# Kernel tuning notes

Hardware: AMD Instinct MI355X
Metric: run time of the kernel (lower is better)

## Reference

```python
import jax, jax.numpy as jnp
import numpy as np

B, D, H = 4096, 32, 1024  # batch, in_out_dim, hidden width


def setup_inputs() -> dict:
    key = jax.random.key(0)
    ks = jax.random.split(key, 10)

    def lin_w(k, shape, fan_in):
        bound = 1.0 / np.sqrt(fan_in)
        return jax.random.uniform(k, shape, jnp.float32, -bound, bound)

    return {
        "t": jax.random.uniform(ks[0], (1,), jnp.float32),
        "z": jax.random.normal(ks[1], (B, D), jnp.float32),
        "W0": lin_w(ks[2], (H, D + 1), D + 1),
        "b0": lin_w(ks[3], (H,), D + 1),
        "W1": lin_w(ks[4], (H, H), H),
        "b1": lin_w(ks[5], (H,), H),
        "W2": lin_w(ks[6], (H, H), H),
        "b2": lin_w(ks[7], (H,), H),
        "W3": lin_w(ks[8], (D, H), H),
        "b3": lin_w(ks[9], (D,), H),
    }


def _mlp(v, params):
    # Linear -> Tanh chain, final Linear (torch convention y = x @ W.T + b)
    for W, b in params[:-1]:
        v = jnp.tanh(v @ W.T + b)
    W, b = params[-1]
    return v @ W.T + b


def reference(t, z, W0, b0, W1, b1, W2, b2, W3, b3):
    bsz, d = z.shape
    tt = jnp.broadcast_to(t.reshape(-1), (bsz,))  # check_t: repeat scalar t
    params = [(W0, b0), (W1, b1), (W2, b2), (W3, b3)]

    def f(zz):  # [B, D] -> [B, D]
        v = jnp.concatenate([zz, tt[:, None]], axis=1)  # [B, D+1]
        return _mlp(v, params)

    out = f(z)

    # Exact Jacobian trace via d forward-mode JVPs (replaces the per-dim
    # autograd.grad loop in trace_df_dz with a single vmapped JVP batch).
    eye = jnp.eye(d, dtype=z.dtype)

    def jvp_i(e):
        return jax.jvp(f, (z,), (jnp.broadcast_to(e, z.shape),))[1]  # [B, D]

    tang = jax.vmap(jvp_i)(eye)            # [D, B, D]
    trace = jnp.einsum("ibi->b", tang)     # sum_i df_i/dz_i per sample
    divv = -trace
    return out, divv[:, None]
```

## Files before the change

kernel.cpp:

```cpp
#include <hip/hip_runtime.h>
#include <hip/hip_bf16.h>
#include <stdint.h>


using bf  = __hip_bfloat16;
using bf2 = __hip_bfloat162;
typedef __attribute__((ext_vector_type(8))) short bf16x8;
typedef __attribute__((ext_vector_type(4))) float f32x4;

__device__ __forceinline__ float b2f(bf x)    { return __bfloat162float(x); }
__device__ __forceinline__ bf    f2b(float x) { return __float2bfloat16(x); }

__device__ __forceinline__ void gld16(const void* g, void* l) {
  __builtin_amdgcn_global_load_lds((const __attribute__((address_space(1))) void*)g,
                                   (__attribute__((address_space(3))) void*)l,
                                   16, 0, 0);
}

__device__ __forceinline__ void conv_body(int blk, const float* __restrict__ src,
                                          bf* __restrict__ dst, int n4) {
  const int i = blk * 256 + threadIdx.x;
  if (i >= n4) return;
  float4 v = ((const float4*)src)[i];
  bf2* d = (bf2*)(dst + (size_t)i * 4);
  d[0] = __float22bfloat162_rn(make_float2(v.x, v.y));
  d[1] = __float22bfloat162_rn(make_float2(v.z, v.w));
}

__device__ __forceinline__ void w0t_body(int blk, const float* __restrict__ W0,
                                         bf* __restrict__ W0T) {
  const int idx = blk * 256 + threadIdx.x;
  const int i = idx >> 10, q = idx & 1023;
  W0T[idx] = f2b(W0[q * 33 + i]);
}

__global__ __launch_bounds__(256) void prep_k(const float* __restrict__ z,
                                              const float* __restrict__ tin,
                                              const float* __restrict__ W0,
                                              const float* __restrict__ b0,
                                              const float* __restrict__ W1,
                                              const float* __restrict__ W2,
                                              const float* __restrict__ W3,
                                              bf* __restrict__ h0,
                                              bf* __restrict__ W0T,
                                              bf* __restrict__ W1b,
                                              bf* __restrict__ W2b,
                                              bf* __restrict__ W3b,
                                              float* __restrict__ out2) {
  __shared__ float zs[32 * 33];
  const int f = blockIdx.x, t = threadIdx.x;
  if (f < 128) {
    const int s0 = f * 32;
    for (int j = t; j < 1024; j += 256) {
      const int s = j >> 5, k = j & 31;
      zs[s * 33 + k] = z[(size_t)(s0 + s) * 32 + k];
    }
    if (t < 32) zs[t * 33 + 32] = tin[0];
    __syncthreads();
#pragma unroll 1
    for (int rep = 0; rep < 4; ++rep) {
      const int hh = rep * 256 + t;
      const float* wr = W0 + (size_t)hh * 33;
      float wv[33];
#pragma unroll
      for (int k = 0; k < 33; ++k) wv[k] = wr[k];
      const float bv = b0[hh];
#pragma unroll 1
      for (int s = 0; s < 32; ++s) {
        float acc = bv;
#pragma unroll
        for (int k = 0; k < 33; ++k) acc += wv[k] * zs[s * 33 + k];
        h0[(size_t)(s0 + s) * 1024 + hh] = f2b(tanhf(acc));
      }
    }
  } else if (f < 1152) {
    conv_body(f - 128, W1, W1b, 262144);
  } else if (f < 2176) {
    conv_body(f - 1152, W2, W2b, 262144);
  } else if (f < 2208) {
    conv_body(f - 2176, W3, W3b, 8192);
  } else if (f < 2336) {
    w0t_body(f - 2208, W0, W0T);
  } else {
#pragma unroll
    for (int u = 0; u < 16; ++u) out2[u * 256 + t] = 0.f;
  }
}

__device__ __forceinline__ void gemm_core(bf* As, bf* Bs,
                                          const bf* __restrict__ A,
                                          const bf* __restrict__ B,
                                          size_t m0, size_t n0,
                                          f32x4 (&acc)[8][4]) {
  constexpr int K = 1024;
  const int t = threadIdx.x, l = t & 63, w = t >> 6;
  const int wm = w >> 1, wn = w & 1;
  const int r15 = l & 15, q4 = l >> 4, sw = r15 & 7;

  const int lrow = l >> 3;
  const int lseg = (l & 7) ^ lrow;
  const bf* asrc[8]; bf* alds[8];
  const bf* bsrc[4]; bf* blds[4];
#pragma unroll
  for (int u = 0; u < 8; ++u) {
    const int row = w * 64 + u * 8 + lrow;
    asrc[u] = A + (m0 + row) * K + lseg * 8;
    alds[u] = As + (size_t)(w * 64 + u * 8) * 64;
  }
#pragma unroll
  for (int u = 0; u < 4; ++u) {
    const int row = w * 32 + u * 8 + lrow;
    bsrc[u] = B + (n0 + row) * K + lseg * 8;
    blds[u] = Bs + (size_t)(w * 32 + u * 8) * 64;
  }

#pragma unroll 1
  for (int k0 = 0; k0 < K; k0 += 64) {
#pragma unroll
    for (int u = 0; u < 8; ++u) gld16(asrc[u] + k0, alds[u]);
#pragma unroll
    for (int u = 0; u < 4; ++u) gld16(bsrc[u] + k0, blds[u]);
    __syncthreads();
#pragma unroll
    for (int kk = 0; kk < 2; ++kk) {
      const int sa = (kk * 4 + q4) ^ sw;
      bf16x8 af[8], bfr[4];
#pragma unroll
      for (int i = 0; i < 8; ++i)
        af[i] = *(const bf16x8*)(As + (wm * 128 + i * 16 + r15) * 64 + sa * 8);
#pragma unroll
      for (int j = 0; j < 4; ++j)
        bfr[j] = *(const bf16x8*)(Bs + (wn * 64 + j * 16 + r15) * 64 + sa * 8);
#pragma unroll
      for (int mi = 0; mi < 8; ++mi)
#pragma unroll
        for (int ni = 0; ni < 4; ++ni)
          acc[mi][ni] = __builtin_amdgcn_mfma_f32_16x16x32_bf16(af[mi], bfr[ni], acc[mi][ni], 0, 0, 0);
    }
    __syncthreads();
  }
}

__global__ __launch_bounds__(256, 2) void gemm_fwd(const bf* __restrict__ A,
                                                   const bf* __restrict__ W,
                                                   const float* __restrict__ bias,
                                                   bf* __restrict__ H) {
  constexpr int N = 1024;
  __shared__ __align__(16) bf As[256 * 64];
  __shared__ __align__(16) bf Bs[128 * 64];
  const int t = threadIdx.x, l = t & 63, w = t >> 6;
  const int wm = w >> 1, wn = w & 1;
  const int f = blockIdx.x;
  const int n_t = (f >> 3) & 7, m_t = (f & 7) + 8 * (f >> 6);
  const size_t m0 = (size_t)m_t * 256, n0 = (size_t)n_t * 128;
  const int r15 = l & 15, q4 = l >> 4;
  f32x4 acc[8][4] = {};
  gemm_core(As, Bs, A, W, m0, n0, acc);
#pragma unroll
  for (int ni = 0; ni < 4; ++ni) {
    const int n = (int)n0 + wn * 64 + ni * 16 + r15;
    const float bv = bias[n];
#pragma unroll
    for (int mi = 0; mi < 8; ++mi)
#pragma unroll
      for (int r = 0; r < 4; ++r) {
        const size_t m = m0 + wm * 128 + mi * 16 + q4 * 4 + r;
        H[m * N + n] = f2b(tanhf(acc[mi][ni][r] + bv));
      }
  }
}

__global__ __launch_bounds__(256) void fwd3_k(const bf* __restrict__ h2,
                                              const bf* __restrict__ W3b,
                                              const float* __restrict__ b3,
                                              float* __restrict__ out) {
  __shared__ __align__(16) bf hs[8 * 1024];
  const int t = threadIdx.x;
  const size_t bb = (size_t)blockIdx.x * 8;
  const uint4* src = (const uint4*)(h2 + bb * 1024);
  uint4* dv = (uint4*)hs;
#pragma unroll
  for (int j = 0; j < 4; ++j) dv[j * 256 + t] = src[j * 256 + t];
  __syncthreads();
  const int i = t & 31, bl = t >> 5;
  const bf2* hr = (const bf2*)(hs + bl * 1024);
  const bf2* wr = (const bf2*)(W3b + (size_t)i * 1024);
  float s = 0.f;
#pragma unroll 8
  for (int k2 = 0; k2 < 512; ++k2) {
    float2 a = __bfloat1622float2(hr[k2]);
    float2 c = __bfloat1622float2(wr[k2]);
    s += a.x * c.x + a.y * c.y;
  }
  out[(bb + bl) * 32 + i] = s + b3[i];
}

__global__ __launch_bounds__(256) void t0_k(const bf* __restrict__ h0c,
                                            const bf* __restrict__ W0T,
                                            bf* __restrict__ T0) {
  const int idx = blockIdx.x * 256 + threadIdx.x;
  const int m = idx >> 6, seg = idx & 63;
  const int b = m >> 5, i = m & 31;
  const bf2* hp = (const bf2*)(h0c + (size_t)b * 1024 + seg * 16);
  const bf2* wp = (const bf2*)(W0T + (size_t)i * 1024 + seg * 16);
  bf2* dp = (bf2*)(T0 + (size_t)m * 1024 + seg * 16);
#pragma unroll
  for (int u = 0; u < 8; ++u) {
    float2 h = __bfloat1622float2(hp[u]);
    float2 w = __bfloat1622float2(wp[u]);
    float2 r;
    r.x = (1.f - h.x * h.x) * w.x;
    r.y = (1.f - h.y * h.y) * w.y;
    dp[u] = __float22bfloat162_rn(r);
  }
}

__global__ __launch_bounds__(256, 2) void gemm_jvp1(const bf* __restrict__ T0,
                                                    const bf* __restrict__ W1b,
                                                    const bf* __restrict__ h1c,
                                                    bf* __restrict__ T1) {
  constexpr int N = 1024;
  __shared__ __align__(16) bf As[256 * 64];
  __shared__ __align__(16) bf Bs[128 * 64];
  const int t = threadIdx.x, l = t & 63, w = t >> 6;
  const int wm = w >> 1, wn = w & 1;
  const int f = blockIdx.x;
  const int n_t = (f >> 3) & 7, m_t = (f & 7) + 8 * (f >> 6);
  const size_t m0 = (size_t)m_t * 256, n0 = (size_t)n_t * 128;
  const int r15 = l & 15, q4 = l >> 4;
  f32x4 acc[8][4] = {};
  gemm_core(As, Bs, T0, W1b, m0, n0, acc);
  const int bbase = (int)((m0 + wm * 128) >> 5);
#pragma unroll
  for (int ni = 0; ni < 4; ++ni) {
    const int n = (int)n0 + wn * 64 + ni * 16 + r15;
    float a1v[4];
#pragma unroll
    for (int s = 0; s < 4; ++s) {
      const float hv = b2f(h1c[(size_t)(bbase + s) * 1024 + n]);
      a1v[s] = 1.f - hv * hv;
    }
#pragma unroll
    for (int mi = 0; mi < 8; ++mi)
#pragma unroll
      for (int r = 0; r < 4; ++r) {
        const size_t m = m0 + wm * 128 + mi * 16 + q4 * 4 + r;
        T1[m * N + n] = f2b(a1v[mi >> 1] * acc[mi][ni][r]);
      }
  }
}

__global__ __launch_bounds__(256, 2) void gemm_jvp2(const bf* __restrict__ T1,
                                                    const bf* __restrict__ W2b,
                                                    const bf* __restrict__ W3b,
                                                    const bf* __restrict__ h2c,
                                                    float* __restrict__ out2c) {
  __shared__ __align__(16) bf As[256 * 64];
  __shared__ __align__(16) bf Bs[128 * 64];
  const int t = threadIdx.x, l = t & 63, w = t >> 6;
  const int wm = w >> 1, wn = w & 1;
  const int f = blockIdx.x;
  const int n_t = (f >> 3) & 7, m_t = (f & 7) + 8 * (f >> 6);
  const size_t m0 = (size_t)m_t * 256, n0 = (size_t)n_t * 128;
  const int r15 = l & 15, q4 = l >> 4;
  f32x4 acc[8][4] = {};
  gemm_core(As, Bs, T1, W2b, m0, n0, acc);
  const int bbase = (int)((m0 + wm * 128) >> 5);
  float part[4] = {0.f, 0.f, 0.f, 0.f};
#pragma unroll
  for (int ni = 0; ni < 4; ++ni) {
    const int n = (int)n0 + wn * 64 + ni * 16 + r15;
    float a2v[4];
#pragma unroll
    for (int s = 0; s < 4; ++s) {
      const float hv = b2f(h2c[(size_t)(bbase + s) * 1024 + n]);
      a2v[s] = 1.f - hv * hv;
    }
#pragma unroll
    for (int mi = 0; mi < 8; ++mi) {
      const int isel = mi >> 1;
#pragma unroll
      for (int r = 0; r < 4; ++r) {
        const int mm = wm * 128 + mi * 16 + q4 * 4 + r;
        part[isel] += b2f(W3b[(size_t)(mm & 31) * 1024 + n]) * a2v[isel] * acc[mi][ni][r];
      }
    }
  }
#pragma unroll
  for (int off = 32; off > 0; off >>= 1) {
#pragma unroll
    for (int s = 0; s < 4; ++s) part[s] += __shfl_down(part[s], off);
  }
  if (l == 0) {
#pragma unroll
    for (int s = 0; s < 4; ++s) atomicAdd(out2c + bbase + s, -part[s]);
  }
}

extern "C" void kernel_launch(void* const* d_in, const int* in_sizes, int n_in,
                              void* d_out, int out_size, void* d_ws, size_t ws_size,
                              hipStream_t stream) {
  const float* tin = (const float*)d_in[0];
  const float* z   = (const float*)d_in[1];
  const float* W0  = (const float*)d_in[2];
  const float* b0  = (const float*)d_in[3];
  const float* W1  = (const float*)d_in[4];
  const float* b1  = (const float*)d_in[5];
  const float* W2  = (const float*)d_in[6];
  const float* b2  = (const float*)d_in[7];
  const float* W3  = (const float*)d_in[8];
  const float* b3  = (const float*)d_in[9];
  float* out = (float*)d_out;
  float* out2 = out + 131072;
  (void)in_sizes; (void)n_in; (void)out_size;

  char* ws = (char*)d_ws;
  size_t off = 0;
  auto take = [&](size_t bytes) {
    char* p = ws + off;
    off = (off + bytes + 255) & ~(size_t)255;
    return p;
  };
  bf* h0   = (bf*)take((size_t)4096 * 1024 * 2);
  bf* h1   = (bf*)take((size_t)4096 * 1024 * 2);
  bf* h2   = (bf*)take((size_t)4096 * 1024 * 2);
  bf* W0T  = (bf*)take((size_t)32 * 1024 * 2);
  bf* W1b  = (bf*)take((size_t)1024 * 1024 * 2);
  bf* W2b  = (bf*)take((size_t)1024 * 1024 * 2);
  bf* W3b  = (bf*)take((size_t)32 * 1024 * 2);
  const size_t avail = (ws_size > off) ? (ws_size - off) : 0;
  int NB = 4096;
  while (NB > 256 && 2 * (size_t)NB * 65536 > avail) NB >>= 1;
  bf* T0 = (bf*)take((size_t)NB * 65536);
  bf* T1 = (bf*)take((size_t)NB * 65536);

  prep_k<<<dim3(2337), dim3(256), 0, stream>>>(z, tin, W0, b0, W1, W2, W3,
                                               h0, W0T, W1b, W2b, W3b, out2);
  gemm_fwd<<<dim3(128), dim3(256), 0, stream>>>(h0, W1b, b1, h1);
  gemm_fwd<<<dim3(128), dim3(256), 0, stream>>>(h1, W2b, b2, h2);
  fwd3_k<<<dim3(512), dim3(256), 0, stream>>>(h2, W3b, b3, out);
  for (int cb = 0; cb < 4096; cb += NB) {
    t0_k<<<dim3(NB * 8), dim3(256), 0, stream>>>(h0 + (size_t)cb * 1024, W0T, T0);
    gemm_jvp1<<<dim3(NB), dim3(256), 0, stream>>>(
        T0, W1b, h1 + (size_t)cb * 1024, T1);
    gemm_jvp2<<<dim3(NB), dim3(256), 0, stream>>>(
        T1, W2b, W3b, h2 + (size_t)cb * 1024, out2 + cb);
  }
}
```

Baseline: 819.6 us.

## Software-pipeline JVP chunks in one fused launch and shrink forward GEMM tiles

```diff
diff --git a/kernel.cpp b/kernel.cpp
--- a/kernel.cpp
+++ b/kernel.cpp
@@ -32,6 +32,26 @@
   const int idx = blk * 256 + threadIdx.x;
   const int i = idx >> 10, q = idx & 1023;
   W0T[idx] = f2b(W0[q * 33 + i]);
+}
+
+__device__ __forceinline__ void t0_body(int blk, const bf* __restrict__ h0c,
+                                        const bf* __restrict__ W0T,
+                                        bf* __restrict__ T0) {
+  const int idx = blk * 256 + threadIdx.x;
+  const int m = idx >> 6, seg = idx & 63;
+  const int b = m >> 5, i = m & 31;
+  const bf2* hp = (const bf2*)(h0c + (size_t)b * 1024 + seg * 16);
+  const bf2* wp = (const bf2*)(W0T + (size_t)i * 1024 + seg * 16);
+  bf2* dp = (bf2*)(T0 + (size_t)m * 1024 + seg * 16);
+#pragma unroll
+  for (int u = 0; u < 8; ++u) {
+    float2 h = __bfloat1622float2(hp[u]);
+    float2 w = __bfloat1622float2(wp[u]);
+    float2 r;
+    r.x = (1.f - h.x * h.x) * w.x;
+    r.y = (1.f - h.y * h.y) * w.y;
+    dp[u] = __float22bfloat162_rn(r);
+  }
 }
 
 __global__ __launch_bounds__(256) void prep_k(const float* __restrict__ z,
@@ -87,18 +107,18 @@
   }
 }
 
-__device__ __forceinline__ void gemm_core(bf* As, bf* Bs,
-                                          const bf* __restrict__ A,
-                                          const bf* __restrict__ B,
-                                          size_t m0, size_t n0,
-                                          f32x4 (&acc)[8][4]) {
+
+__device__ __forceinline__ void gemm_core256(bf* As, bf* Bs,
+                                             const bf* __restrict__ A,
+                                             const bf* __restrict__ B,
+                                             size_t m0, size_t n0,
+                                             f32x4 (&acc)[8][4]) {
   constexpr int K = 1024;
   const int t = threadIdx.x, l = t & 63, w = t >> 6;
   const int wm = w >> 1, wn = w & 1;
   const int r15 = l & 15, q4 = l >> 4, sw = r15 & 7;
-
-  const int lrow = l >> 3;
-  const int lseg = (l & 7) ^ lrow;
+  const int lrow = l >> 3, lseg = (l & 7) ^ lrow;
+
   const bf* asrc[8]; bf* alds[8];
   const bf* bsrc[4]; bf* blds[4];
 #pragma unroll
@@ -133,6 +153,52 @@
         bfr[j] = *(const bf16x8*)(Bs + (wn * 64 + j * 16 + r15) * 64 + sa * 8);
 #pragma unroll
       for (int mi = 0; mi < 8; ++mi)
+#pragma unroll
+        for (int ni = 0; ni < 4; ++ni)
+          acc[mi][ni] = __builtin_amdgcn_mfma_f32_16x16x32_bf16(af[mi], bfr[ni], acc[mi][ni], 0, 0, 0);
+    }
+    __syncthreads();
+  }
+}
+
+__device__ __forceinline__ void gemm_core128(bf* As, bf* Bs,
+                                             const bf* __restrict__ A,
+                                             const bf* __restrict__ B,
+                                             size_t m0, size_t n0,
+                                             f32x4 (&acc)[4][4]) {
+  constexpr int K = 1024;
+  const int t = threadIdx.x, l = t & 63, w = t >> 6;
+  const int wm = w >> 1, wn = w & 1;
+  const int r15 = l & 15, q4 = l >> 4, sw = r15 & 7;
+  const int lrow = l >> 3, lseg = (l & 7) ^ lrow;
+
+  const bf* asrc[4]; bf* alds[4];
+  const bf* bsrc[4]; bf* blds[4];
+#pragma unroll
+  for (int u = 0; u < 4; ++u) {
+    const int row = w * 32 + u * 8 + lrow;
+    asrc[u] = A + (m0 + row) * K + lseg * 8;
+    alds[u] = As + (size_t)(w * 32 + u * 8) * 64;
+    bsrc[u] = B + (n0 + row) * K + lseg * 8;
+    blds[u] = Bs + (size_t)(w * 32 + u * 8) * 64;
+  }
+
+#pragma unroll 1
+  for (int k0 = 0; k0 < K; k0 += 64) {
+#pragma unroll
+    for (int u = 0; u < 4; ++u) { gld16(asrc[u] + k0, alds[u]); gld16(bsrc[u] + k0, blds[u]); }
+    __syncthreads();
+#pragma unroll
+    for (int kk = 0; kk < 2; ++kk) {
+      const int sa = (kk * 4 + q4) ^ sw;
+      bf16x8 af[4], bfr[4];
+#pragma unroll
+      for (int i = 0; i < 4; ++i) {
+        af[i]  = *(const bf16x8*)(As + (wm * 64 + i * 16 + r15) * 64 + sa * 8);
+        bfr[i] = *(const bf16x8*)(Bs + (wn * 64 + i * 16 + r15) * 64 + sa * 8);
+      }
+#pragma unroll
+      for (int mi = 0; mi < 4; ++mi)
 #pragma unroll
         for (int ni = 0; ni < 4; ++ni)
           acc[mi][ni] = __builtin_amdgcn_mfma_f32_16x16x32_bf16(af[mi], bfr[ni], acc[mi][ni], 0, 0, 0);
@@ -146,25 +212,25 @@
                                                    const float* __restrict__ bias,
                                                    bf* __restrict__ H) {
   constexpr int N = 1024;
-  __shared__ __align__(16) bf As[256 * 64];
+  __shared__ __align__(16) bf As[128 * 64];
   __shared__ __align__(16) bf Bs[128 * 64];
   const int t = threadIdx.x, l = t & 63, w = t >> 6;
   const int wm = w >> 1, wn = w & 1;
   const int f = blockIdx.x;
   const int n_t = (f >> 3) & 7, m_t = (f & 7) + 8 * (f >> 6);
-  const size_t m0 = (size_t)m_t * 256, n0 = (size_t)n_t * 128;
+  const size_t m0 = (size_t)m_t * 128, n0 = (size_t)n_t * 128;
   const int r15 = l & 15, q4 = l >> 4;
-  f32x4 acc[8][4] = {};
-  gemm_core(As, Bs, A, W, m0, n0, acc);
+  f32x4 acc[4][4] = {};
+  gemm_core128(As, Bs, A, W, m0, n0, acc);
 #pragma unroll
   for (int ni = 0; ni < 4; ++ni) {
     const int n = (int)n0 + wn * 64 + ni * 16 + r15;
     const float bv = bias[n];
 #pragma unroll
-    for (int mi = 0; mi < 8; ++mi)
+    for (int mi = 0; mi < 4; ++mi)
 #pragma unroll
       for (int r = 0; r < 4; ++r) {
-        const size_t m = m0 + wm * 128 + mi * 16 + q4 * 4 + r;
+        const size_t m = m0 + wm * 64 + mi * 16 + q4 * 4 + r;
         H[m * N + n] = f2b(tanhf(acc[mi][ni][r] + bv));
       }
   }
@@ -198,102 +264,89 @@
 __global__ __launch_bounds__(256) void t0_k(const bf* __restrict__ h0c,
                                             const bf* __restrict__ W0T,
                                             bf* __restrict__ T0) {
-  const int idx = blockIdx.x * 256 + threadIdx.x;
-  const int m = idx >> 6, seg = idx & 63;
-  const int b = m >> 5, i = m & 31;
-  const bf2* hp = (const bf2*)(h0c + (size_t)b * 1024 + seg * 16);
-  const bf2* wp = (const bf2*)(W0T + (size_t)i * 1024 + seg * 16);
-  bf2* dp = (bf2*)(T0 + (size_t)m * 1024 + seg * 16);
-#pragma unroll
-  for (int u = 0; u < 8; ++u) {
-    float2 h = __bfloat1622float2(hp[u]);
-    float2 w = __bfloat1622float2(wp[u]);
-    float2 r;
-    r.x = (1.f - h.x * h.x) * w.x;
-    r.y = (1.f - h.y * h.y) * w.y;
-    dp[u] = __float22bfloat162_rn(r);
-  }
-}
-
-__global__ __launch_bounds__(256, 2) void gemm_jvp1(const bf* __restrict__ T0,
-                                                    const bf* __restrict__ W1b,
-                                                    const bf* __restrict__ h1c,
-                                                    bf* __restrict__ T1) {
-  constexpr int N = 1024;
-  __shared__ __align__(16) bf As[256 * 64];
-  __shared__ __align__(16) bf Bs[128 * 64];
+  t0_body(blockIdx.x, h0c, W0T, T0);
+}
+
+__global__ __launch_bounds__(256, 2) void jvp_step_k(
+    const bf* __restrict__ T1p, const bf* __restrict__ h2p,
+    float* __restrict__ out2p,
+    const bf* __restrict__ T0c, const bf* __restrict__ h1c,
+    bf* __restrict__ T1c,
+    const bf* __restrict__ h0n, bf* __restrict__ T0n,
+    const bf* __restrict__ W1b, const bf* __restrict__ W2b,
+    const bf* __restrict__ W3b, const bf* __restrict__ W0T,
+    int n2, int n1) {
+  __shared__ __align__(16) bf smem[24576];
+  const int f = blockIdx.x;
   const int t = threadIdx.x, l = t & 63, w = t >> 6;
   const int wm = w >> 1, wn = w & 1;
-  const int f = blockIdx.x;
-  const int n_t = (f >> 3) & 7, m_t = (f & 7) + 8 * (f >> 6);
+  const int r15 = l & 15, q4 = l >> 4;
+
+  if (f >= n2 + n1) {
+    t0_body(f - n2 - n1, h0n, W0T, T0n);
+    return;
+  }
+  int ff, fam;
+  if (n2 > 0 && n1 > 0) { ff = f >> 1; fam = f & 1; }
+  else if (n2 > 0)      { ff = f; fam = 0; }
+  else                  { ff = f; fam = 1; }
+  const int n_t = (ff >> 3) & 7, m_t = (ff & 7) + 8 * (ff >> 6);
   const size_t m0 = (size_t)m_t * 256, n0 = (size_t)n_t * 128;
-  const int r15 = l & 15, q4 = l >> 4;
-  f32x4 acc[8][4] = {};
-  gemm_core(As, Bs, T0, W1b, m0, n0, acc);
-  const int bbase = (int)((m0 + wm * 128) >> 5);
-#pragma unroll
-  for (int ni = 0; ni < 4; ++ni) {
-    const int n = (int)n0 + wn * 64 + ni * 16 + r15;
-    float a1v[4];
-#pragma unroll
-    for (int s = 0; s < 4; ++s) {
-      const float hv = b2f(h1c[(size_t)(bbase + s) * 1024 + n]);
-      a1v[s] = 1.f - hv * hv;
-    }
-#pragma unroll
-    for (int mi = 0; mi < 8; ++mi)
-#pragma unroll
-      for (int r = 0; r < 4; ++r) {
-        const size_t m = m0 + wm * 128 + mi * 16 + q4 * 4 + r;
-        T1[m * N + n] = f2b(a1v[mi >> 1] * acc[mi][ni][r]);
-      }
-  }
-}
-
-__global__ __launch_bounds__(256, 2) void gemm_jvp2(const bf* __restrict__ T1,
-                                                    const bf* __restrict__ W2b,
-                                                    const bf* __restrict__ W3b,
-                                                    const bf* __restrict__ h2c,
-                                                    float* __restrict__ out2c) {
-  __shared__ __align__(16) bf As[256 * 64];
-  __shared__ __align__(16) bf Bs[128 * 64];
-  const int t = threadIdx.x, l = t & 63, w = t >> 6;
-  const int wm = w >> 1, wn = w & 1;
-  const int f = blockIdx.x;
-  const int n_t = (f >> 3) & 7, m_t = (f & 7) + 8 * (f >> 6);
-  const size_t m0 = (size_t)m_t * 256, n0 = (size_t)n_t * 128;
-  const int r15 = l & 15, q4 = l >> 4;
-  f32x4 acc[8][4] = {};
-  gemm_core(As, Bs, T1, W2b, m0, n0, acc);
-  const int bbase = (int)((m0 + wm * 128) >> 5);
-  float part[4] = {0.f, 0.f, 0.f, 0.f};
-#pragma unroll
-  for (int ni = 0; ni < 4; ++ni) {
-    const int n = (int)n0 + wn * 64 + ni * 16 + r15;
-    float a2v[4];
-#pragma unroll
-    for (int s = 0; s < 4; ++s) {
-      const float hv = b2f(h2c[(size_t)(bbase + s) * 1024 + n]);
-      a2v[s] = 1.f - hv * hv;
-    }
-#pragma unroll
-    for (int mi = 0; mi < 8; ++mi) {
-      const int isel = mi >> 1;
-#pragma unroll
-      for (int r = 0; r < 4; ++r) {
-        const int mm = wm * 128 + mi * 16 + q4 * 4 + r;
-        part[isel] += b2f(W3b[(size_t)(mm & 31) * 1024 + n]) * a2v[isel] * acc[mi][ni][r];
-      }
-    }
-  }
-#pragma unroll
-  for (int off = 32; off > 0; off >>= 1) {
-#pragma unroll
-    for (int s = 0; s < 4; ++s) part[s] += __shfl_down(part[s], off);
-  }
-  if (l == 0) {
-#pragma unroll
-    for (int s = 0; s < 4; ++s) atomicAdd(out2c + bbase + s, -part[s]);
+
+  if (fam == 0) {
+    f32x4 acc[8][4] = {};
+    gemm_core256(smem, smem + 16384, T1p, W2b, m0, n0, acc);
+    const int bbase = (int)((m0 + wm * 128) >> 5);
+    float part[4] = {0.f, 0.f, 0.f, 0.f};
+#pragma unroll
+    for (int ni = 0; ni < 4; ++ni) {
+      const int n = (int)n0 + wn * 64 + ni * 16 + r15;
+      float a2v[4];
+#pragma unroll
+      for (int s = 0; s < 4; ++s) {
+        const float hv = b2f(h2p[(size_t)(bbase + s) * 1024 + n]);
+        a2v[s] = 1.f - hv * hv;
+      }
+#pragma unroll
+      for (int mi = 0; mi < 8; ++mi) {
+        const int isel = mi >> 1;
+#pragma unroll
+        for (int r = 0; r < 4; ++r) {
+          const int mm = wm * 128 + mi * 16 + q4 * 4 + r;
+          part[isel] += b2f(W3b[(size_t)(mm & 31) * 1024 + n]) * a2v[isel] * acc[mi][ni][r];
+        }
+      }
+    }
+#pragma unroll
+    for (int off2 = 32; off2 > 0; off2 >>= 1) {
+#pragma unroll
+      for (int s = 0; s < 4; ++s) part[s] += __shfl_down(part[s], off2);
+    }
+    if (l == 0) {
+#pragma unroll
+      for (int s = 0; s < 4; ++s) atomicAdd(out2p + bbase + s, -part[s]);
+    }
+  } else {
+    f32x4 acc[8][4] = {};
+    gemm_core256(smem, smem + 16384, T0c, W1b, m0, n0, acc);
+    const int bbase = (int)((m0 + wm * 128) >> 5);
+#pragma unroll
+    for (int ni = 0; ni < 4; ++ni) {
+      const int n = (int)n0 + wn * 64 + ni * 16 + r15;
+      float a1v[4];
+#pragma unroll
+      for (int s = 0; s < 4; ++s) {
+        const float hv = b2f(h1c[(size_t)(bbase + s) * 1024 + n]);
+        a1v[s] = 1.f - hv * hv;
+      }
+#pragma unroll
+      for (int mi = 0; mi < 8; ++mi)
+#pragma unroll
+        for (int r = 0; r < 4; ++r) {
+          const size_t m = m0 + wm * 128 + mi * 16 + q4 * 4 + r;
+          T1c[m * 1024 + n] = f2b(a1v[mi >> 1] * acc[mi][ni][r]);
+        }
+    }
   }
 }
 
@@ -329,21 +382,42 @@
   bf* W2b  = (bf*)take((size_t)1024 * 1024 * 2);
   bf* W3b  = (bf*)take((size_t)32 * 1024 * 2);
   const size_t avail = (ws_size > off) ? (ws_size - off) : 0;
-  int NB = 4096;
-  while (NB > 256 && 2 * (size_t)NB * 65536 > avail) NB >>= 1;
-  bf* T0 = (bf*)take((size_t)NB * 65536);
-  bf* T1 = (bf*)take((size_t)NB * 65536);
+  int NB = 1024;
+  while (NB > 256 && 4 * (size_t)NB * 65536 > avail) NB >>= 1;
+  bf* T0a = (bf*)take((size_t)NB * 65536);
+  bf* T0b = (bf*)take((size_t)NB * 65536);
+  bf* T1a = (bf*)take((size_t)NB * 65536);
+  bf* T1b = (bf*)take((size_t)NB * 65536);
+  bf* T0buf[2] = {T0a, T0b};
+  bf* T1buf[2] = {T1a, T1b};
+  const int nchunk = 4096 / NB;
 
   prep_k<<<dim3(2337), dim3(256), 0, stream>>>(z, tin, W0, b0, W1, W2, W3,
                                                h0, W0T, W1b, W2b, W3b, out2);
-  gemm_fwd<<<dim3(128), dim3(256), 0, stream>>>(h0, W1b, b1, h1);
-  gemm_fwd<<<dim3(128), dim3(256), 0, stream>>>(h1, W2b, b2, h2);
+  gemm_fwd<<<dim3(256), dim3(256), 0, stream>>>(h0, W1b, b1, h1);
+  gemm_fwd<<<dim3(256), dim3(256), 0, stream>>>(h1, W2b, b2, h2);
   fwd3_k<<<dim3(512), dim3(256), 0, stream>>>(h2, W3b, b3, out);
-  for (int cb = 0; cb < 4096; cb += NB) {
-    t0_k<<<dim3(NB * 8), dim3(256), 0, stream>>>(h0 + (size_t)cb * 1024, W0T, T0);
-    gemm_jvp1<<<dim3(NB), dim3(256), 0, stream>>>(
-        T0, W1b, h1 + (size_t)cb * 1024, T1);
-    gemm_jvp2<<<dim3(NB), dim3(256), 0, stream>>>(
-        T1, W2b, W3b, h2 + (size_t)cb * 1024, out2 + cb);
-  }
-}
+  t0_k<<<dim3(NB * 8), dim3(256), 0, stream>>>(h0, W0T, T0buf[0]);
+
+  for (int s = 0; s <= nchunk; ++s) {
+    const int c2 = s - 1, c1 = s, c0 = s + 1;
+    const int n2 = (c2 >= 0 && c2 < nchunk) ? NB : 0;
+    const int n1 = (c1 < nchunk) ? NB : 0;
+    const int nt = (c0 < nchunk) ? NB * 8 : 0;
+    if (n2 + n1 + nt == 0) continue;
+    const int c2c = (c2 >= 0) ? c2 : 0;
+    const int c1c = (c1 < nchunk) ? c1 : 0;
+    const int c0c = (c0 < nchunk) ? c0 : 0;
+    const bf* T1p = T1buf[c2c & 1];
+    const bf* h2p = h2 + (size_t)c2c * NB * 1024;
+    float* o2p    = out2 + (size_t)c2c * NB;
+    const bf* T0c = T0buf[c1c & 1];
+    const bf* h1c = h1 + (size_t)c1c * NB * 1024;
+    bf* T1c = T1buf[c1c & 1];
+    const bf* h0n = h0 + (size_t)c0c * NB * 1024;
+    bf* T0n = T0buf[c0c & 1];
+    jvp_step_k<<<dim3(n2 + n1 + nt), dim3(256), 0, stream>>>(
+        T1p, h2p, o2p, T0c, h1c, T1c, h0n, T0n,
+        W1b, W2b, W3b, W0T, n2, n1);
+  }
+}
```

New measurement: 825.3 us. No clear change (+0.7%).
